# Performance work log

Measured on AMD Instinct MI355X. Metric: run time of the kernel, lower is better.

## Reference

```python
import jax, jax.numpy as jnp
import numpy as np

# Static diagonal offsets of the SparseDIA matrix (eqx static field).
OFFSETS = (-128, -64, -8, -1, 0, 1, 8, 64, 128)
N = 8192   # matrix dimension (diags.shape[1])
M = 4096   # number of dense columns in `other`


def setup_inputs() -> dict:
    key = jax.random.key(0)
    k1, k2 = jax.random.split(key)
    diags = jax.random.normal(k1, (len(OFFSETS), N), dtype=jnp.float32)
    other = jax.random.normal(k2, (N, M), dtype=jnp.float32)
    return {"diags": diags, "other": other}


def reference(diags, other):
    """SparseDIA._matmul_dense(left_matmul=True): out = A_dia @ other.

    For each static offset k, rows [top:bottom] of the output accumulate
    diag[start:end] (the valid part of the stored diagonal) times the
    matching rows of `other`. Offsets are Python ints, so all slices are
    static and jit-compatible.
    """
    n = other.shape[0]
    out = jnp.zeros_like(other)
    for k, offset in enumerate(OFFSETS):
        start = max(0, offset)
        end = min(n, n + offset)
        top = max(0, -offset)
        bottom = top + (end - start)
        out = out.at[top:bottom, :].add(
            diags[k, start:end, None] * other[start:end, :]
        )
    return out
```

## Files before the change

### kernel.cpp

```cpp
#include <hip/hip_runtime.h>


#define DIA_N   8192
#define DIA_M   4096
#define M4      (DIA_M / 4)
#define CB      8
#define BR      64
#define HALO    128
#define RING    512
#define NB      32
#define GROUP   (BR * NB)
#define THREADS 512

typedef float f4 __attribute__((ext_vector_type(4)));
typedef __attribute__((address_space(3))) unsigned int       lds_uint;
typedef const __attribute__((address_space(1))) unsigned int glb_uint;

__global__ __launch_bounds__(THREADS, 4) void sparse_dia_kernel(
    const float* __restrict__ diags,
    const float* __restrict__ other,
    float* __restrict__ out)
{
    constexpr int OFF[9] = {-128, -64, -8, -1, 0, 1, 8, 64, 128};

    __shared__ f4 ring[RING][CB];

    const int tid  = threadIdx.x;
    const int gr0  = blockIdx.y * GROUP;
    const int cb4  = blockIdx.x * CB;

    const int wave = tid >> 6;
    const int lane = tid & 63;
    const int lrow = lane >> 3;
    const int lcol = lane & 7;
    const int scol = lcol ^ lrow;

    const int c = tid & 7;
    const int i = tid >> 3;

    f4* __restrict__ out4 = (f4*)out;

    auto gll8 = [&](int slot0, int q0) {
        int q = q0 + lrow;
        q = (q < 0) ? 0 : (q >= DIA_N ? DIA_N - 1 : q);
        const float* src = other + ((size_t)q * DIA_M + (size_t)(cb4 + scol) * 4);
        __builtin_amdgcn_global_load_lds((glb_uint*)src,
            (lds_uint*)&ring[slot0][0], 16, 0, 0);
    };

    auto load_diag = [&](int t, float (&dk)[9]) {
        const int b = gr0 + t * BR + i;
        if (gr0 + t * BR - HALO >= 0 && gr0 + t * BR + (BR - 1) + HALO < DIA_N) {
#pragma unroll
            for (int k = 0; k < 9; ++k)
                dk[k] = diags[k * DIA_N + b + OFF[k]];
        } else {
#pragma unroll
            for (int k = 0; k < 9; ++k) {
                const int q  = b + OFF[k];
                const int qc = (q < 0) ? 0 : (q >= DIA_N ? DIA_N - 1 : q);
                const float v = diags[k * DIA_N + qc];
                dk[k] = ((unsigned)q < (unsigned)DIA_N) ? v : 0.f;
            }
        }
    };

    auto compute_store = [&](int t, const float (&dk)[9]) {
        const int L0 = t * BR + HALO + i;
        f4 a = (f4){0.f, 0.f, 0.f, 0.f};
#pragma unroll
        for (int k = 0; k < 9; ++k) {
            const int s = (L0 + OFF[k]) & (RING - 1);
            a += dk[k] * ring[s][c ^ (s & 7)];
        }
        out4[(size_t)(gr0 + t * BR + i) * M4 + cb4 + c] = a;
    };

    float dkA[9], dkB[9];

#pragma unroll
    for (int s = 0; s < 5; ++s) {
        const int inst = wave * 5 + s;
        gll8(inst * 8, gr0 - HALO + inst * 8);
    }
    gll8(320 + wave * 8, gr0 - HALO + 320 + wave * 8);
    load_diag(0, dkA);
    load_diag(1, dkB);
    asm volatile("s_waitcnt vmcnt(0)" ::: "memory");
    __builtin_amdgcn_s_barrier();
    __builtin_amdgcn_sched_barrier(0);

    auto body = [&](int t, float (&dk)[9]) {
        const int Lc = t * BR + 384;
        gll8((Lc & (RING - 1)) + wave * 8, gr0 - HALO + Lc + wave * 8);
        compute_store(t, dk);
        load_diag(t + 2, dk);
        asm volatile("s_waitcnt vmcnt(11)" ::: "memory");
        __builtin_amdgcn_s_barrier();
        __builtin_amdgcn_sched_barrier(0);
    };

    for (int t = 0; t < NB - 2; t += 2) {
        body(t,     dkA);
        body(t + 1, dkB);
    }

    compute_store(NB - 2, dkA);
    asm volatile("s_waitcnt vmcnt(1)" ::: "memory");
    __builtin_amdgcn_s_barrier();
    __builtin_amdgcn_sched_barrier(0);
    compute_store(NB - 1, dkB);
}

extern "C" void kernel_launch(void* const* d_in, const int* in_sizes, int n_in,
                              void* d_out, int out_size, void* d_ws, size_t ws_size,
                              hipStream_t stream) {
    const float* diags = (const float*)d_in[0];
    const float* other = (const float*)d_in[1];
    float* out         = (float*)d_out;

    dim3 block(THREADS, 1, 1);
    dim3 grid(M4 / CB, DIA_N / GROUP, 1);
    sparse_dia_kernel<<<grid, block, 0, stream>>>(diags, other, out);
}
```

Before: 247.9 us.

## Give each wave a private LDS ring column and drop block barriers

Each wave now owns one f4 column and streams 64 rows per load into its own LDS ring, so the block-wide s_barrier calls are removed and waits rely only on per-wave vmcnt. The XOR swizzle goes away because each wave's ring is a contiguous 1-D array. The cost is a less coalesced global access pattern: each lane reads 16 bytes from a different row, which spreads a wave's traffic over 64 rows instead of a few contiguous row segments. Diag loads are also replicated across the waves of a block.

After: 345.9 us. 1.4x slower.

```diff
diff --git a/kernel.cpp b/kernel.cpp
--- a/kernel.cpp
+++ b/kernel.cpp
@@ -4,13 +4,13 @@
 #define DIA_N   8192
 #define DIA_M   4096
 #define M4      (DIA_M / 4)
-#define CB      8
 #define BR      64
 #define HALO    128
 #define RING    512
 #define NB      32
 #define GROUP   (BR * NB)
 #define THREADS 512
+#define NWAVES  (THREADS / 64)
 
 typedef float f4 __attribute__((ext_vector_type(4)));
 typedef __attribute__((address_space(3))) unsigned int       lds_uint;
@@ -23,41 +23,38 @@
 {
     constexpr int OFF[9] = {-128, -64, -8, -1, 0, 1, 8, 64, 128};
 
-    __shared__ f4 ring[RING][CB];
+    __shared__ f4 ring[NWAVES][RING];
 
     const int tid  = threadIdx.x;
-    const int gr0  = blockIdx.y * GROUP;
-    const int cb4  = blockIdx.x * CB;
-
     const int wave = tid >> 6;
     const int lane = tid & 63;
-    const int lrow = lane >> 3;
-    const int lcol = lane & 7;
-    const int scol = lcol ^ lrow;
 
-    const int c = tid & 7;
-    const int i = tid >> 3;
+    const int gr0  = blockIdx.y * GROUP;
+    const int col4 = blockIdx.x * NWAVES + wave;
 
-    f4* __restrict__ out4 = (f4*)out;
+    const f4* __restrict__ o4   = (const f4*)other;
+    f4* __restrict__       out4 = (f4*)out;
 
-    auto gll8 = [&](int slot0, int q0) {
-        int q = q0 + lrow;
+    auto gll64 = [&](int m) {
+        int q = gr0 - HALO + m * BR + lane;
         q = (q < 0) ? 0 : (q >= DIA_N ? DIA_N - 1 : q);
-        const float* src = other + ((size_t)q * DIA_M + (size_t)(cb4 + scol) * 4);
+        const float* src = (const float*)&o4[(size_t)q * M4 + col4];
         __builtin_amdgcn_global_load_lds((glb_uint*)src,
-            (lds_uint*)&ring[slot0][0], 16, 0, 0);
+            (lds_uint*)&ring[wave][(m * BR) & (RING - 1)], 16, 0, 0);
     };
 
     auto load_diag = [&](int t, float (&dk)[9]) {
-        const int b = gr0 + t * BR + i;
-        if (gr0 + t * BR - HALO >= 0 && gr0 + t * BR + (BR - 1) + HALO < DIA_N) {
+        const int r  = gr0 + t * BR + lane;
+        const int lo = gr0 + t * BR - HALO;
+        const int hi = gr0 + t * BR + (BR - 1) + HALO;
+        if (lo >= 0 && hi < DIA_N) {
 #pragma unroll
             for (int k = 0; k < 9; ++k)
-                dk[k] = diags[k * DIA_N + b + OFF[k]];
+                dk[k] = diags[k * DIA_N + r + OFF[k]];
         } else {
 #pragma unroll
             for (int k = 0; k < 9; ++k) {
-                const int q  = b + OFF[k];
+                const int q  = r + OFF[k];
                 const int qc = (q < 0) ? 0 : (q >= DIA_N ? DIA_N - 1 : q);
                 const float v = diags[k * DIA_N + qc];
                 dk[k] = ((unsigned)q < (unsigned)DIA_N) ? v : 0.f;
@@ -66,38 +63,29 @@
     };
 
     auto compute_store = [&](int t, const float (&dk)[9]) {
-        const int L0 = t * BR + HALO + i;
+        const int L0 = t * BR + HALO + lane;
         f4 a = (f4){0.f, 0.f, 0.f, 0.f};
 #pragma unroll
-        for (int k = 0; k < 9; ++k) {
-            const int s = (L0 + OFF[k]) & (RING - 1);
-            a += dk[k] * ring[s][c ^ (s & 7)];
-        }
-        out4[(size_t)(gr0 + t * BR + i) * M4 + cb4 + c] = a;
+        for (int k = 0; k < 9; ++k)
+            a += dk[k] * ring[wave][(L0 + OFF[k]) & (RING - 1)];
+        out4[(size_t)(gr0 + t * BR + lane) * M4 + col4] = a;
     };
 
     float dkA[9], dkB[9];
 
 #pragma unroll
-    for (int s = 0; s < 5; ++s) {
-        const int inst = wave * 5 + s;
-        gll8(inst * 8, gr0 - HALO + inst * 8);
-    }
-    gll8(320 + wave * 8, gr0 - HALO + 320 + wave * 8);
+    for (int m = 0; m < 6; ++m) gll64(m);
     load_diag(0, dkA);
     load_diag(1, dkB);
     asm volatile("s_waitcnt vmcnt(0)" ::: "memory");
-    __builtin_amdgcn_s_barrier();
     __builtin_amdgcn_sched_barrier(0);
 
     auto body = [&](int t, float (&dk)[9]) {
-        const int Lc = t * BR + 384;
-        gll8((Lc & (RING - 1)) + wave * 8, gr0 - HALO + Lc + wave * 8);
+        gll64(t + 6);
+        asm volatile("s_waitcnt vmcnt(12)" ::: "memory");
+        __builtin_amdgcn_sched_barrier(0);
         compute_store(t, dk);
         load_diag(t + 2, dk);
-        asm volatile("s_waitcnt vmcnt(11)" ::: "memory");
-        __builtin_amdgcn_s_barrier();
-        __builtin_amdgcn_sched_barrier(0);
     };
 
     for (int t = 0; t < NB - 2; t += 2) {
@@ -105,10 +93,9 @@
         body(t + 1, dkB);
     }
 
+    asm volatile("s_waitcnt vmcnt(0)" ::: "memory");
+    __builtin_amdgcn_sched_barrier(0);
     compute_store(NB - 2, dkA);
-    asm volatile("s_waitcnt vmcnt(1)" ::: "memory");
-    __builtin_amdgcn_s_barrier();
-    __builtin_amdgcn_sched_barrier(0);
     compute_store(NB - 1, dkB);
 }
 
@@ -120,6 +107,6 @@
     float* out         = (float*)d_out;
 
     dim3 block(THREADS, 1, 1);
-    dim3 grid(M4 / CB, DIA_N / GROUP, 1);
+    dim3 grid(M4 / NWAVES, DIA_N / GROUP, 1);
     sparse_dia_kernel<<<grid, block, 0, stream>>>(diags, other, out);
 }
```

## Double block size and deepen ring pipeline with triple-buffered diagonal prefetch

Applied to the files above, without the earlier changes.

Doubles the rows per step and threads per block to 1024 and the LDS ring to 1024 rows, so each block covers 4096 rows with fewer blocks along the row dimension. The staging of `other` runs five chunks ahead and the diagonal coefficients are prefetched three steps ahead using four rotating register sets, with the wait count relaxed. The aim is to hide global latency better and amortize barriers, at the cost of larger blocks, more LDS per block and more registers, which can lower occupancy and grid parallelism. The loop now also stages and loads past the end of the block, using clamped addresses.

Result: no change. 246.6 us (-0.5%).

```diff
diff --git a/kernel.cpp b/kernel.cpp
--- a/kernel.cpp
+++ b/kernel.cpp
@@ -5,25 +5,25 @@
 #define DIA_M   4096
 #define M4      (DIA_M / 4)
 #define CB      8
-#define BR      64
+#define BR      128
 #define HALO    128
-#define RING    512
+#define RINGR   1024
 #define NB      32
 #define GROUP   (BR * NB)
-#define THREADS 512
+#define THREADS 1024
 
 typedef float f4 __attribute__((ext_vector_type(4)));
 typedef __attribute__((address_space(3))) unsigned int       lds_uint;
 typedef const __attribute__((address_space(1))) unsigned int glb_uint;
 
-__global__ __launch_bounds__(THREADS, 4) void sparse_dia_kernel(
+__global__ __launch_bounds__(THREADS) void sparse_dia_kernel(
     const float* __restrict__ diags,
     const float* __restrict__ other,
     float* __restrict__ out)
 {
     constexpr int OFF[9] = {-128, -64, -8, -1, 0, 1, 8, 64, 128};
 
-    __shared__ f4 ring[RING][CB];
+    __shared__ f4 ring[RINGR][CB];
 
     const int tid  = threadIdx.x;
     const int gr0  = blockIdx.y * GROUP;
@@ -38,26 +38,30 @@
     const int c = tid & 7;
     const int i = tid >> 3;
 
-    f4* __restrict__ out4 = (f4*)out;
+    const f4* __restrict__ o4   = (const f4*)other;
+    f4* __restrict__       out4 = (f4*)out;
 
-    auto gll8 = [&](int slot0, int q0) {
-        int q = q0 + lrow;
+    auto stage_chunk = [&](int m) {
+        const int L = BR * m + 8 * wave;
+        int q = gr0 - HALO + L + lrow;
         q = (q < 0) ? 0 : (q >= DIA_N ? DIA_N - 1 : q);
-        const float* src = other + ((size_t)q * DIA_M + (size_t)(cb4 + scol) * 4);
+        const float* src = (const float*)&o4[(size_t)q * M4 + cb4 + scol];
         __builtin_amdgcn_global_load_lds((glb_uint*)src,
-            (lds_uint*)&ring[slot0][0], 16, 0, 0);
+            (lds_uint*)&ring[L & (RINGR - 1)][0], 16, 0, 0);
     };
 
     auto load_diag = [&](int t, float (&dk)[9]) {
-        const int b = gr0 + t * BR + i;
-        if (gr0 + t * BR - HALO >= 0 && gr0 + t * BR + (BR - 1) + HALO < DIA_N) {
+        const int r  = gr0 + t * BR + i;
+        const int lo = gr0 + t * BR - HALO;
+        const int hi = gr0 + t * BR + (BR - 1) + HALO;
+        if (lo >= 0 && hi < DIA_N) {
 #pragma unroll
             for (int k = 0; k < 9; ++k)
-                dk[k] = diags[k * DIA_N + b + OFF[k]];
+                dk[k] = diags[k * DIA_N + r + OFF[k]];
         } else {
 #pragma unroll
             for (int k = 0; k < 9; ++k) {
-                const int q  = b + OFF[k];
+                const int q  = r + OFF[k];
                 const int qc = (q < 0) ? 0 : (q >= DIA_N ? DIA_N - 1 : q);
                 const float v = diags[k * DIA_N + qc];
                 dk[k] = ((unsigned)q < (unsigned)DIA_N) ? v : 0.f;
@@ -66,50 +70,43 @@
     };
 
     auto compute_store = [&](int t, const float (&dk)[9]) {
-        const int L0 = t * BR + HALO + i;
+        const int L0 = HALO + t * BR + i;
         f4 a = (f4){0.f, 0.f, 0.f, 0.f};
 #pragma unroll
         for (int k = 0; k < 9; ++k) {
-            const int s = (L0 + OFF[k]) & (RING - 1);
+            const int s = (L0 + OFF[k]) & (RINGR - 1);
             a += dk[k] * ring[s][c ^ (s & 7)];
         }
         out4[(size_t)(gr0 + t * BR + i) * M4 + cb4 + c] = a;
     };
 
-    float dkA[9], dkB[9];
+    auto body = [&](int t, const float (&use)[9], float (&ld)[9]) {
+        stage_chunk(t + 5);
+        load_diag(t + 3, ld);
+        asm volatile("s_waitcnt vmcnt(33)" ::: "memory");
+        __builtin_amdgcn_sched_barrier(0);
+        __builtin_amdgcn_s_barrier();
+        __builtin_amdgcn_sched_barrier(0);
+        compute_store(t, use);
+    };
+
+    float d0[9], d1[9], d2[9], d3[9];
 
 #pragma unroll
-    for (int s = 0; s < 5; ++s) {
-        const int inst = wave * 5 + s;
-        gll8(inst * 8, gr0 - HALO + inst * 8);
-    }
-    gll8(320 + wave * 8, gr0 - HALO + 320 + wave * 8);
-    load_diag(0, dkA);
-    load_diag(1, dkB);
+    for (int m = 0; m < 5; ++m) stage_chunk(m);
+    load_diag(0, d0);
+    load_diag(1, d1);
+    load_diag(2, d2);
     asm volatile("s_waitcnt vmcnt(0)" ::: "memory");
     __builtin_amdgcn_s_barrier();
     __builtin_amdgcn_sched_barrier(0);
 
-    auto body = [&](int t, float (&dk)[9]) {
-        const int Lc = t * BR + 384;
-        gll8((Lc & (RING - 1)) + wave * 8, gr0 - HALO + Lc + wave * 8);
-        compute_store(t, dk);
-        load_diag(t + 2, dk);
-        asm volatile("s_waitcnt vmcnt(11)" ::: "memory");
-        __builtin_amdgcn_s_barrier();
-        __builtin_amdgcn_sched_barrier(0);
-    };
-
-    for (int t = 0; t < NB - 2; t += 2) {
-        body(t,     dkA);
-        body(t + 1, dkB);
+    for (int t = 0; t < NB; t += 4) {
+        body(t,     d0, d3);
+        body(t + 1, d1, d0);
+        body(t + 2, d2, d1);
+        body(t + 3, d3, d2);
     }
-
-    compute_store(NB - 2, dkA);
-    asm volatile("s_waitcnt vmcnt(1)" ::: "memory");
-    __builtin_amdgcn_s_barrier();
-    __builtin_amdgcn_sched_barrier(0);
-    compute_store(NB - 1, dkB);
 }
 
 extern "C" void kernel_launch(void* const* d_in, const int* in_sizes, int n_in,
```
